# Performance work log

Measured on AMD Instinct MI355X. Metric: run time of the kernel, lower is better.

The kernel has to match this reference:

```python
import jax, jax.numpy as jnp
import numpy as np

B, N, D = 16, 1369, 1024
HID, NH = 512, 8
SCALE = np.sqrt(D // NH)


def _pos_encoding_2d(n, d):
    ps = int(np.sqrt(n))  # 37; n is a perfect square here
    div = jnp.exp(jnp.arange(0, d // 2, 2, dtype=jnp.float32) * (-np.log(10000.0) / (d // 2)))
    rows = (jnp.arange(n) // ps).astype(jnp.float32)
    cols = (jnp.arange(n) % ps).astype(jnp.float32)
    def interleave(s, c):
        return jnp.stack([s, c], axis=-1).reshape(n, -1)
    half_row = interleave(jnp.sin(rows[:, None] * div), jnp.cos(rows[:, None] * div))
    half_col = interleave(jnp.sin(cols[:, None] * div), jnp.cos(cols[:, None] * div))
    return jnp.concatenate([half_row, half_col], axis=-1)  # [n, d]


def _center_bias(n, strength=0.3):
    ps = int(np.sqrt(n))
    c = ps // 2
    y, x = jnp.meshgrid(jnp.arange(ps, dtype=jnp.float32), jnp.arange(ps, dtype=jnp.float32), indexing='ij')
    d2 = (x - c) ** 2 + (y - c) ** 2
    sigma = ps / 6.0
    return (jnp.exp(-d2 / (2.0 * sigma ** 2)).reshape(-1)) * strength  # [n]


def setup_inputs() -> dict:
    key = jax.random.key(0)
    ks = jax.random.split(key, 16)
    s = 0.02
    return {
        'patch_tokens': jax.random.normal(ks[0], (B, N, D), dtype=jnp.float32),
        'curiosity_score': jax.random.uniform(ks[1], (B,), dtype=jnp.float32),
        'Wq': jax.random.normal(ks[2], (D, D), dtype=jnp.float32) * s,
        'bq': jax.random.uniform(ks[3], (D,), minval=-0.05, maxval=0.05, dtype=jnp.float32),
        'Wk': jax.random.normal(ks[4], (D, D), dtype=jnp.float32) * s,
        'bk': jax.random.uniform(ks[5], (D,), minval=-0.05, maxval=0.05, dtype=jnp.float32),
        'Wv': jax.random.normal(ks[6], (D, D), dtype=jnp.float32) * s,
        'bv': jnp.zeros((D,), dtype=jnp.float32),
        'Wc1': jax.random.normal(ks[7], (1, HID // 8), dtype=jnp.float32) * s,
        'bc1': jnp.zeros((HID // 8,), dtype=jnp.float32),
        'Wc2': jax.random.normal(ks[8], (HID // 8, NH), dtype=jnp.float32) * s,
        'bc2': jnp.zeros((NH,), dtype=jnp.float32),
        'Wp1': jax.random.normal(ks[9], (D, HID), dtype=jnp.float32) * s,
        'bp1': jnp.zeros((HID,), dtype=jnp.float32),
        'Wp2': jax.random.normal(ks[10], (HID, HID // 4), dtype=jnp.float32) * s,
        'bp2': jnp.zeros((HID // 4,), dtype=jnp.float32),
        'adaptive_weight': jnp.float32(0.5),
    }


def reference(patch_tokens, curiosity_score, Wq, bq, Wk, bk, Wv, bv,
              Wc1, bc1, Wc2, bc2, Wp1, bp1, Wp2, bp2, adaptive_weight):
    b, n, d = patch_tokens.shape
    x = patch_tokens + _pos_encoding_2d(n, d)[None]  # [B,N,D]

    q = x @ Wq + bq
    k = x @ Wk + bk
    v = x @ Wv + bv

    scores = jnp.einsum('bqd,bkd->bqk', q, k) / SCALE          # [B,N,N]
    attn = jax.nn.softmax(scores, axis=-1)                     # dropout p=0 / eval
    attended = jnp.einsum('bqk,bkd->bqd', attn, v)             # [B,N,D]

    cb = _center_bias(n)[None]                                 # [1,N]
    VAR_EPS = 1e-6

    pa = attn.mean(axis=1) + cb
    # fallback chain (data-dependent in torch; expressed with jnp.where)
    pa2 = jnp.diagonal(attn, axis1=-2, axis2=-1) + cb
    pa = jnp.where(jnp.var(pa, ddof=1) < VAR_EPS, pa2, pa)
    pa3 = attn.max(axis=-1) + cb
    pa = jnp.where(jnp.var(pa, ddof=1) < VAR_EPS, pa3, pa)
    norms = jnp.linalg.norm(x, axis=-1)
    noise = jax.random.normal(jax.random.key(42), norms.shape, dtype=norms.dtype) * 0.1 * jnp.std(norms, ddof=1)
    pa = jnp.where(jnp.var(pa, ddof=1) < VAR_EPS, norms + noise, pa)

    pa = pa / (pa.sum(axis=-1, keepdims=True) + 1e-8)

    # curiosity modulation
    h = jax.nn.relu(curiosity_score[:, None] @ Wc1 + bc1)
    cm = jax.nn.sigmoid(h @ Wc2 + bc2)                         # [B,NH]
    cw = cm.mean(axis=-1, keepdims=True)                       # [B,1]
    modulated = pa * (1.0 + cw)
    fa = adaptive_weight * modulated + (1.0 - adaptive_weight) * pa

    fa = jnp.clip(fa, 1e-8, None)
    fa = fa / (fa.sum(axis=-1, keepdims=True) + 1e-8)

    weighted = jnp.sum(attended * fa[..., None], axis=1)       # [B,D]
    focal = jax.nn.relu(weighted @ Wp1 + bp1) @ Wp2 + bp2      # [B,HID//4]
    return focal, fa
```

## Files before the change

kernel.cpp:

```cpp
#include <hip/hip_runtime.h>
#include <hip/hip_bf16.h>
#include <cstdint>

#define B_   16
#define N_   1369
#define NP   1536
#define D_   1024
#define NQK  2048
#define SLD  1568
#define QLD  2080

typedef __bf16 bf16x8_t __attribute__((ext_vector_type(8)));
typedef __bf16 bf16x4_t __attribute__((ext_vector_type(4)));
typedef float  f32x4_t  __attribute__((ext_vector_type(4)));

__device__ __forceinline__ float  bf2f(__bf16 x) { return (float)x; }
__device__ __forceinline__ __bf16 f2bf(float x)  { return (__bf16)x; }

#define GLOAD_LDS16(g, l) __builtin_amdgcn_global_load_lds( \
    (const __attribute__((address_space(1))) void*)(g),     \
    (__attribute__((address_space(3))) void*)(l), 16, 0, 0)

__global__ __launch_bounds__(256)
void pos_kernel(float* __restrict__ pos)
{
    const int idx = blockIdx.x * 256 + threadIdx.x;
    if (idx >= N_ * D_) return;
    const int n = idx >> 10, f = idx & 1023;
    const int row = n / 37, col = n - row * 37;
    const float base = (f < 512) ? (float)row : (float)col;
    const int  t2   = (f & 511) >> 1;
    const float dv  = __expf(-0.03597789207803197f * (float)t2);
    const float ang = base * dv;
    pos[idx] = (f & 1) ? cosf(ang) : sinf(ang);
}

__global__ __launch_bounds__(256)
void addpos_kernel(const float* __restrict__ patch, const float* __restrict__ pos,
                   __bf16* __restrict__ X)
{
    const long tid = (long)blockIdx.x * 256 + threadIdx.x;
    const long e   = tid * 4;
    const int  f   = (int)(e & 1023);
    const long nb  = e >> 10;
    const int  n   = (int)(nb % NP);
    const long b   = nb / NP;
    bf16x4_t o;
    if (n < N_) {
        const float4 p = *(const float4*)(patch + ((b * N_ + n) << 10) + f);
        const float4 q = *(const float4*)(pos + ((long)n << 10) + f);
        o[0] = f2bf(p.x + q.x); o[1] = f2bf(p.y + q.y);
        o[2] = f2bf(p.z + q.z); o[3] = f2bf(p.w + q.w);
    } else {
        o[0] = o[1] = o[2] = o[3] = f2bf(0.f);
    }
    *(bf16x4_t*)(X + e) = o;
}

__global__ __launch_bounds__(256)
void wcast_kernel(const float* __restrict__ W0, const float* __restrict__ W1,
                  __bf16* __restrict__ T0, __bf16* __restrict__ T1)
{
    const float* W = blockIdx.z == 0 ? W0 : W1;
    __bf16*      T = blockIdx.z == 0 ? T0 : T1;
    __shared__ float tile[64][65];
    const int o0 = blockIdx.x * 64, i0 = blockIdx.y * 64;
    const int t = threadIdx.x;
    const int tr = t >> 4, tc = (t & 15) * 4;
    #pragma unroll
    for (int rr = 0; rr < 64; rr += 16) {
        float4 v = *(const float4*)(W + (long)(i0 + rr + tr) * 1024 + o0 + tc);
        tile[rr + tr][tc + 0] = v.x; tile[rr + tr][tc + 1] = v.y;
        tile[rr + tr][tc + 2] = v.z; tile[rr + tr][tc + 3] = v.w;
    }
    __syncthreads();
    #pragma unroll
    for (int rr = 0; rr < 64; rr += 16) {
        bf16x4_t o;
        o[0] = f2bf(tile[tc + 0][rr + tr]); o[1] = f2bf(tile[tc + 1][rr + tr]);
        o[2] = f2bf(tile[tc + 2][rr + tr]); o[3] = f2bf(tile[tc + 3][rr + tr]);
        *(bf16x4_t*)(T + (long)(o0 + rr + tr) * 1024 + i0 + tc) = o;
    }
}

__global__ __launch_bounds__(256)
void bcat_kernel(const float* __restrict__ bq, const float* __restrict__ bk,
                 float* __restrict__ bcat)
{
    const int i = blockIdx.x * 256 + threadIdx.x;
    if (i >= NQK) return;
    bcat[i] = (i < 1024) ? bq[i] : bk[i - 1024];
}

template<int HAS_BIAS, int STATS>
__device__ __forceinline__
void gemm_body(const __bf16* __restrict__ A, const __bf16* __restrict__ Bt,
               __bf16* __restrict__ C, const float* __restrict__ bias,
               float2* __restrict__ mzp,
               int lda, int ldb, int ldc, int Kd, float scale,
               long sA, long sB, long sC, int tilesN, int tilesPerBatch, int cpx)
{
    __shared__ __bf16 lds[65536];
    const int bid = blockIdx.x;
    const int vt  = (bid & 7) * cpx + (bid >> 3);
    const int bz  = vt / tilesPerBatch;
    const int rem = vt - bz * tilesPerBatch;
    const int ty  = rem / tilesN;
    const int tx  = rem - ty * tilesN;
    A  += (long)bz * sA;  Bt += (long)bz * sB;  C += (long)bz * sC;
    const int m0 = ty * 256, n0 = tx * 256;

    const int t  = threadIdx.x;
    const int w  = t >> 6, l = t & 63;
    const int wr = w >> 2, wc = w & 3;
    const int lr = l & 15, lh = l >> 4;

    const int laneF  = (lr * 64 + ((lh * 16) ^ (((lr >> 3) & 1) << 5))) >> 1;
    const int rstage = (w >> 1) * 16 + (l >> 2);
    const int kstage = (w & 1) * 32 + (((l & 3) * 8) ^ (((l >> 5) & 1) << 4));

    const __bf16* Ag = A  + (long)(m0 + rstage) * lda + kstage;
    const __bf16* Bg = Bt + (long)(n0 + rstage) * ldb + kstage;
    __bf16* dA = lds + w * 512;
    __bf16* dB = lds + 16384 + w * 512;

#define SA_(buf, half, kt) GLOAD_LDS16(Ag + (long)(half) * 128 * lda + (kt) * 64, \
                                       dA + (buf) * 32768 + (half) * 8192)
#define SB_(buf, half, kt) GLOAD_LDS16(Bg + (long)(half) * 128 * ldb + (kt) * 64, \
                                       dB + (buf) * 32768 + (half) * 8192)

    f32x4_t acc[4][4] = {};

    const int NT = Kd >> 6;
    SA_(0, 0, 0); SA_(0, 1, 0); SB_(0, 0, 0); SB_(0, 1, 0);
    asm volatile("s_waitcnt vmcnt(0)" ::: "memory");
    __builtin_amdgcn_s_barrier();

    for (int tk = 0; tk < NT; ++tk) {
        const int c = tk & 1, o = c ^ 1;
        if (tk + 1 < NT) {
            SA_(o, 0, tk + 1); SA_(o, 1, tk + 1);
            SB_(o, 0, tk + 1); SB_(o, 1, tk + 1);
        }
        const int cb = c * 32768;
        const __bf16* ap = lds + cb + (wr >> 1) * 8192 + (wr & 1) * 4096 + laneF;
        const __bf16* bp = lds + cb + 16384 + (wc >> 1) * 8192 + (wc & 1) * 4096 + laneF;
        bf16x8_t af[4], bfm[4];
        #pragma unroll
        for (int nn = 0; nn < 4; ++nn) bfm[nn] = *(const bf16x8_t*)(bp + nn * 1024);
        #pragma unroll
        for (int mi = 0; mi < 4; ++mi) af[mi]  = *(const bf16x8_t*)(ap + mi * 1024);
        __builtin_amdgcn_s_setprio(1);
        #pragma unroll
        for (int mi = 0; mi < 4; ++mi)
            #pragma unroll
            for (int nn = 0; nn < 4; ++nn)
                acc[mi][nn] = __builtin_amdgcn_mfma_f32_16x16x32_bf16(af[mi], bfm[nn], acc[mi][nn], 0, 0, 0);
        __builtin_amdgcn_s_setprio(0);
        #pragma unroll
        for (int nn = 0; nn < 4; ++nn) bfm[nn] = *(const bf16x8_t*)(bp + nn * 1024 + 512);
        #pragma unroll
        for (int mi = 0; mi < 4; ++mi) af[mi]  = *(const bf16x8_t*)(ap + mi * 1024 + 512);
        __builtin_amdgcn_s_setprio(1);
        #pragma unroll
        for (int mi = 0; mi < 4; ++mi)
            #pragma unroll
            for (int nn = 0; nn < 4; ++nn)
                acc[mi][nn] = __builtin_amdgcn_mfma_f32_16x16x32_bf16(af[mi], bfm[nn], acc[mi][nn], 0, 0, 0);
        __builtin_amdgcn_s_setprio(0);
        asm volatile("s_waitcnt vmcnt(0)" ::: "memory");
        __builtin_amdgcn_s_barrier();
    }

    #pragma unroll
    for (int mi = 0; mi < 4; ++mi) {
        const int row = m0 + wr * 64 + mi * 16 + lh * 4;
        #pragma unroll
        for (int nn = 0; nn < 4; ++nn) {
            const int col = n0 + wc * 64 + nn * 16 + lr;
            const float bb = HAS_BIAS ? bias[col] : 0.0f;
            #pragma unroll
            for (int q = 0; q < 4; ++q) {
                if (!STATS || ((row + q) < N_ && col < N_))
                    C[(long)(row + q) * ldc + col] = f2bf(acc[mi][nn][q] * scale + bb);
            }
        }
    }

    if (STATS) {
        __syncthreads();
        float* lm = (float*)lds;
        float* lz = lm + 1024;
        #pragma unroll
        for (int mi = 0; mi < 4; ++mi) {
            #pragma unroll
            for (int qq = 0; qq < 4; ++qq) {
                float vb[4]; float m = -3.0e38f;
                #pragma unroll
                for (int nn = 0; nn < 4; ++nn) {
                    const int col = n0 + wc * 64 + nn * 16 + lr;
                    const float vr = bf2f(f2bf(acc[mi][nn][qq] * scale));
                    vb[nn] = (col < N_) ? vr : -3.0e38f;
                    m = fmaxf(m, vb[nn]);
                }
                #pragma unroll
                for (int o = 1; o <= 8; o <<= 1) m = fmaxf(m, __shfl_xor(m, o));
                float z = 0.f;
                #pragma unroll
                for (int nn = 0; nn < 4; ++nn) z += __expf(vb[nn] - m);
                #pragma unroll
                for (int o = 1; o <= 8; o <<= 1) z += __shfl_xor(z, o);
                if (lr == 0) {
                    const int r = wr * 64 + mi * 16 + lh * 4 + qq;
                    lm[r * 4 + wc] = m; lz[r * 4 + wc] = z;
                }
            }
        }
        __syncthreads();
        if (t < 256) {
            const float ma = lm[t * 4 + 0], mb = lm[t * 4 + 1];
            const float mc = lm[t * 4 + 2], md = lm[t * 4 + 3];
            const float M = fmaxf(fmaxf(ma, mb), fmaxf(mc, md));
            const float Z = lz[t * 4 + 0] * __expf(ma - M) + lz[t * 4 + 1] * __expf(mb - M)
                          + lz[t * 4 + 2] * __expf(mc - M) + lz[t * 4 + 3] * __expf(md - M);
            mzp[((long)bz * NP + ty * 256 + t) * 6 + tx] = make_float2(M, Z);
        }
    }
#undef SA_
#undef SB_
}

__global__ __launch_bounds__(1024, 4)
void gemm_qk(const __bf16* A, const __bf16* Bt, __bf16* C, const float* bias,
             int lda, int ldb, int ldc, int Kd,
             int tilesN, int tilesPerBatch, int cpx)
{
    gemm_body<1, 0>(A, Bt, C, bias, nullptr, lda, ldb, ldc, Kd, 1.0f,
                    0, 0, 0, tilesN, tilesPerBatch, cpx);
}

__global__ __launch_bounds__(1024, 4)
void gemm_sc(const __bf16* A, const __bf16* Bt, __bf16* C, float2* mzp,
             int lda, int ldb, int ldc, int Kd, float scale,
             long sA, long sB, long sC, int tilesN, int tilesPerBatch, int cpx)
{
    gemm_body<0, 1>(A, Bt, C, nullptr, mzp, lda, ldb, ldc, Kd, scale,
                    sA, sB, sC, tilesN, tilesPerBatch, cpx);
}

template<int WEIGHTED>
__global__ __launch_bounds__(256)
void colsum_kernel(const __bf16* __restrict__ attn, const float2* __restrict__ mzp,
                   const float* __restrict__ wv, float* __restrict__ out)
{
    const int t  = threadIdx.x;
    const int b  = blockIdx.y;
    const int q0 = blockIdx.x * 16;
    __shared__ float sM[16], sZi[16];
    if (t < 16) {
        const int q = q0 + t;
        float M = -3.0e38f, Zi = 1.f;
        if (q < N_) {
            float2 p[6];
            #pragma unroll
            for (int k = 0; k < 6; ++k) { p[k] = mzp[((long)b * NP + q) * 6 + k]; M = fmaxf(M, p[k].x); }
            float Z = 0.f;
            #pragma unroll
            for (int k = 0; k < 6; ++k) Z += p[k].y * __expf(p[k].x - M);
            Zi = 1.f / Z;
        }
        sM[t] = M; sZi[t] = Zi;
    }
    __syncthreads();
    const int k8 = t * 8;
    if (k8 < N_) {
        const int q1 = (q0 + 16 < N_) ? q0 + 16 : N_;
        float s[8] = {};
        const __bf16* base = attn + (long)b * NP * SLD + k8;
        for (int q = q0; q < q1; ++q) {
            bf16x8_t v = *(const bf16x8_t*)(base + (long)q * SLD);
            const float Mq = sM[q - q0];
            float wq = sZi[q - q0];
            if (WEIGHTED) wq *= wv[b * NP + q];
            #pragma unroll
            for (int i = 0; i < 8; ++i) s[i] += wq * __expf(bf2f(v[i]) - Mq);
        }
        #pragma unroll
        for (int i = 0; i < 8; ++i) atomicAdd(out + b * NP + k8 + i, s[i]);
    }
}

__global__ __launch_bounds__(256)
void fa_kernel(const float* __restrict__ pa_raw, const float* __restrict__ curiosity,
               const float* __restrict__ Wc1, const float* __restrict__ bc1,
               const float* __restrict__ Wc2, const float* __restrict__ bc2,
               const float* __restrict__ aw_p,
               float* __restrict__ fa_ws, float* __restrict__ out_fa)
{
    const int b = blockIdx.x, t = threadIdx.x;
    __shared__ float hsh[64];
    __shared__ float red[8];
    __shared__ float cwsh;
    if (t < 64) hsh[t] = fmaxf(0.f, curiosity[b] * Wc1[t] + bc1[t]);
    __syncthreads();
    if (t < 8) {
        float a = bc2[t];
        for (int j = 0; j < 64; ++j) a += hsh[j] * Wc2[j * 8 + t];
        red[t] = 1.f / (1.f + __expf(-a));
    }
    __syncthreads();
    if (t == 0) {
        float cw = 0.f;
        for (int i = 0; i < 8; ++i) cw += red[i];
        cwsh = cw * 0.125f;
    }
    __syncthreads();
    const float aw   = aw_p[0];
    const float modf = 1.f + aw * cwsh;
    const float sig  = 37.f / 6.f;
    const float inv2s2 = 1.f / (2.f * sig * sig);
    float pv[6];
    float s1 = 0.f;
    #pragma unroll
    for (int i = 0; i < 6; ++i) {
        const int k = t + i * 256;
        float p = 0.f;
        if (k < N_) {
            const int y = k / 37, x = k - y * 37;
            const float d2 = (float)((x - 18) * (x - 18) + (y - 18) * (y - 18));
            const float cb = 0.3f * __expf(-d2 * inv2s2);
            p = pa_raw[b * NP + k] * (1.f / 1369.f) + cb;
        }
        pv[i] = p; s1 += p;
    }
    #pragma unroll
    for (int o = 32; o; o >>= 1) s1 += __shfl_xor(s1, o);
    __syncthreads();
    if (!(t & 63)) red[t >> 6] = s1;
    __syncthreads();
    s1 = red[0] + red[1] + red[2] + red[3];
    const float inv1 = 1.f / (s1 + 1e-8f);
    float s2 = 0.f;
    #pragma unroll
    for (int i = 0; i < 6; ++i) {
        const int k = t + i * 256;
        if (k < N_) {
            const float f = fmaxf(pv[i] * inv1 * modf, 1e-8f);
            pv[i] = f; s2 += f;
        }
    }
    #pragma unroll
    for (int o = 32; o; o >>= 1) s2 += __shfl_xor(s2, o);
    if (!(t & 63)) red[4 + (t >> 6)] = s2;
    __syncthreads();
    s2 = red[4] + red[5] + red[6] + red[7];
    const float inv2 = 1.f / (s2 + 1e-8f);
    #pragma unroll
    for (int i = 0; i < 6; ++i) {
        const int k = t + i * 256;
        if (k < N_) {
            const float f = pv[i] * inv2;
            fa_ws[b * NP + k]  = f;
            out_fa[b * N_ + k] = f;
        }
    }
}

__global__ __launch_bounds__(256)
void u_kernel(const float* __restrict__ g, const __bf16* __restrict__ X,
              float* __restrict__ u, float* __restrict__ gsum)
{
    const int b  = blockIdx.y;
    const int k0 = blockIdx.x * 86;
    const int k1 = (k0 + 86 < N_) ? k0 + 86 : N_;
    const int d  = threadIdx.x * 4;
    float a0 = 0, a1 = 0, a2 = 0, a3 = 0, gs = 0;
    const __bf16* xb = X + (long)b * NP * D_ + d;
    for (int k = k0; k < k1; ++k) {
        const float gv = g[b * NP + k];
        bf16x4_t xv = *(const bf16x4_t*)(xb + (long)k * D_);
        a0 += gv * bf2f(xv[0]); a1 += gv * bf2f(xv[1]);
        a2 += gv * bf2f(xv[2]); a3 += gv * bf2f(xv[3]);
        gs += gv;
    }
    atomicAdd(u + b * D_ + d + 0, a0);
    atomicAdd(u + b * D_ + d + 1, a1);
    atomicAdd(u + b * D_ + d + 2, a2);
    atomicAdd(u + b * D_ + d + 3, a3);
    if (threadIdx.x == 0) atomicAdd(gsum + b, gs);
}

__global__ __launch_bounds__(256)
void wv_gemv_kernel(const float* __restrict__ u, const float* __restrict__ gsum,
                    const float* __restrict__ Wv, const float* __restrict__ bv,
                    float* __restrict__ wout)
{
    const int dcx = blockIdx.x, b = blockIdx.y;
    const int t = threadIdx.x;
    __shared__ float us[1024];
    #pragma unroll
    for (int i = 0; i < 4; ++i) us[t + i * 256] = u[b * D_ + t + i * 256];
    __syncthreads();
    const int d = dcx * 256 + t;
    float a = gsum[b] * bv[d];
    #pragma unroll 8
    for (int i = 0; i < 1024; ++i) a += us[i] * Wv[(long)i * 1024 + d];
    wout[b * D_ + d] = a;
}

__global__ __launch_bounds__(256)
void focal1_kernel(const float* __restrict__ weighted, const float* __restrict__ Wp1,
                   const float* __restrict__ bp1, float* __restrict__ h)
{
    const int b = blockIdx.y, jc = blockIdx.x;
    const int t = threadIdx.x;
    const int jl = t >> 2, part = t & 3;
    const int j = jc * 64 + jl;
    const float* wb = weighted + b * 1024 + part * 256;
    const float* wp = Wp1 + (long)(part * 256) * 512 + j;
    float a = 0.f;
    #pragma unroll 8
    for (int d = 0; d < 256; ++d) a += wb[d] * wp[(long)d * 512];
    a += __shfl_xor(a, 1);
    a += __shfl_xor(a, 2);
    if (part == 0) h[b * 512 + j] = fmaxf(a + bp1[j], 0.f);
}

__global__ __launch_bounds__(128)
void focal2_kernel(const float* __restrict__ h, const float* __restrict__ Wp2,
                   const float* __restrict__ bp2, float* __restrict__ out)
{
    const int b = blockIdx.x, o = threadIdx.x;
    __shared__ float hs[512];
    for (int i = o; i < 512; i += 128) hs[i] = h[b * 512 + i];
    __syncthreads();
    float a = bp2[o];
    #pragma unroll 8
    for (int j = 0; j < 512; ++j) a += hs[j] * Wp2[j * 128 + o];
    out[b * 128 + o] = a;
}

extern "C" void kernel_launch(void* const* d_in, const int* in_sizes, int n_in,
                              void* d_out, int out_size, void* d_ws, size_t ws_size,
                              hipStream_t stream)
{
    const float* patch     = (const float*)d_in[0];
    const float* curiosity = (const float*)d_in[1];
    const float* Wq  = (const float*)d_in[2];
    const float* bq  = (const float*)d_in[3];
    const float* Wk  = (const float*)d_in[4];
    const float* bk  = (const float*)d_in[5];
    const float* Wv  = (const float*)d_in[6];
    const float* bv  = (const float*)d_in[7];
    const float* Wc1 = (const float*)d_in[8];
    const float* bc1 = (const float*)d_in[9];
    const float* Wc2 = (const float*)d_in[10];
    const float* bc2 = (const float*)d_in[11];
    const float* Wp1 = (const float*)d_in[12];
    const float* bp1 = (const float*)d_in[13];
    const float* Wp2 = (const float*)d_in[14];
    const float* bp2 = (const float*)d_in[15];
    const float* aw  = (const float*)d_in[16];
    float* out = (float*)d_out;

    char* ws = (char*)d_ws;
    size_t off = 0;
    auto alloc = [&](size_t bytes) -> char* {
        char* p = ws + off;
        off += (bytes + 255) & ~(size_t)255;
        return p;
    };
    float*  pos  = (float*) alloc((size_t)N_ * D_ * 4);
    __bf16* X    = (__bf16*)alloc((size_t)B_ * NP * D_ * 2);
    __bf16* WT   = (__bf16*)alloc((size_t)2 * D_ * D_ * 2);
    __bf16* S    = (__bf16*)alloc((size_t)B_ * NP * SLD * 2);
    __bf16* QK   = (__bf16*)alloc((size_t)B_ * NP * QLD * 2);
    float*  pa   = (float*) alloc((size_t)B_ * NP * 4);
    float*  gbuf = (float*) alloc((size_t)B_ * NP * 4);
    float*  ubuf = (float*) alloc((size_t)B_ * D_ * 4);
    float*  gsum = (float*) alloc((size_t)B_ * 4);
    const size_t zbytes = (size_t)((char*)(gsum + B_) - (char*)pa);
    float*  faw  = (float*) alloc((size_t)B_ * NP * 4);
    float*  bcat = (float*) alloc((size_t)NQK * 4);
    float*  hbuf = (float*) alloc((size_t)B_ * 512 * 4);
    float2* mzp  = (float2*)alloc((size_t)B_ * NP * 6 * 8);
    float*  wsum = (float*) alloc((size_t)B_ * D_ * 4);

    (void)hipMemsetAsync(pa, 0, zbytes, stream);

    pos_kernel<<<(N_ * D_ + 255) / 256, 256, 0, stream>>>(pos);
    addpos_kernel<<<(int)((size_t)B_ * NP * D_ / 4 / 256), 256, 0, stream>>>(patch, pos, X);
    {
        dim3 g(16, 16, 2);
        wcast_kernel<<<g, 256, 0, stream>>>(Wq, Wk, WT, WT + D_ * D_);
    }
    bcat_kernel<<<(NQK + 255) / 256, 256, 0, stream>>>(bq, bk, bcat);
    {
        const int nwg = 96 * 8;
        gemm_qk<<<nwg, 1024, 0, stream>>>(X, WT, QK, bcat,
                                          D_, D_, QLD, D_, 8, nwg, nwg / 8);
    }
    {
        const int nwg = 36 * B_;
        gemm_sc<<<nwg, 1024, 0, stream>>>(QK, QK + 1024, S, mzp,
                                          QLD, QLD, SLD, D_,
                                          0.08838834764831845f,
                                          (long)NP * QLD, (long)NP * QLD,
                                          (long)NP * SLD, 6, 36, nwg / 8);
    }
    {
        dim3 g(86, B_);
        colsum_kernel<0><<<g, 256, 0, stream>>>(S, mzp, nullptr, pa);
    }
    fa_kernel<<<B_, 256, 0, stream>>>(pa, curiosity, Wc1, bc1, Wc2, bc2, aw,
                                      faw, out + B_ * 128);
    {
        dim3 g(86, B_);
        colsum_kernel<1><<<g, 256, 0, stream>>>(S, mzp, faw, gbuf);
    }
    {
        dim3 g(16, B_);
        u_kernel<<<g, 256, 0, stream>>>(gbuf, X, ubuf, gsum);
    }
    {
        dim3 g(4, B_);
        wv_gemv_kernel<<<g, 256, 0, stream>>>(ubuf, gsum, Wv, bv, wsum);
    }
    {
        dim3 g(8, B_);
        focal1_kernel<<<g, 256, 0, stream>>>(wsum, Wp1, bp1, hbuf);
    }
    focal2_kernel<<<B_, 128, 0, stream>>>(hbuf, Wp2, bp2, out);
}
```

Baseline: 551.3 us.

## Drop softmax max-subtraction via atomic row sums and halve GEMM K-tile

The score GEMM no longer computes per-tile row max and partition pairs. Instead it accumulates plain exp sums directly into a per-row Z buffer with atomics, and the colsum kernels use exp(v)/Z with no max shift. The GEMM K-step also drops from 64 to 32, which halves LDS use and may allow more blocks per CU. The risk is overflow in exp if scores grow large, since the stable max shift is gone. The smaller K step also doubles the barrier count per output tile.

Result: slower. 567.0 us (+2.9%).

```diff
diff --git a/kernel.cpp b/kernel.cpp
--- a/kernel.cpp
+++ b/kernel.cpp
@@ -96,11 +96,11 @@
 __device__ __forceinline__
 void gemm_body(const __bf16* __restrict__ A, const __bf16* __restrict__ Bt,
                __bf16* __restrict__ C, const float* __restrict__ bias,
-               float2* __restrict__ mzp,
+               float* __restrict__ rowZ,
                int lda, int ldb, int ldc, int Kd, float scale,
                long sA, long sB, long sC, int tilesN, int tilesPerBatch, int cpx)
 {
-    __shared__ __bf16 lds[65536];
+    __shared__ __bf16 lds[32768];
     const int bid = blockIdx.x;
     const int vt  = (bid & 7) * cpx + (bid >> 3);
     const int bz  = vt / tilesPerBatch;
@@ -115,52 +115,36 @@
     const int wr = w >> 2, wc = w & 3;
     const int lr = l & 15, lh = l >> 4;
 
-    const int laneF  = (lr * 64 + ((lh * 16) ^ (((lr >> 3) & 1) << 5))) >> 1;
-    const int rstage = (w >> 1) * 16 + (l >> 2);
-    const int kstage = (w & 1) * 32 + (((l & 3) * 8) ^ (((l >> 5) & 1) << 4));
+    const int laneF  = lr * 32 + ((lh * 8) ^ (((lr >> 3) & 1) << 4));
+    const int rstage = w * 16 + (l >> 2);
+    const int kstage = ((l & 3) * 8) ^ (((l >> 5) & 1) << 4);
 
     const __bf16* Ag = A  + (long)(m0 + rstage) * lda + kstage;
     const __bf16* Bg = Bt + (long)(n0 + rstage) * ldb + kstage;
     __bf16* dA = lds + w * 512;
-    __bf16* dB = lds + 16384 + w * 512;
-
-#define SA_(buf, half, kt) GLOAD_LDS16(Ag + (long)(half) * 128 * lda + (kt) * 64, \
-                                       dA + (buf) * 32768 + (half) * 8192)
-#define SB_(buf, half, kt) GLOAD_LDS16(Bg + (long)(half) * 128 * ldb + (kt) * 64, \
-                                       dB + (buf) * 32768 + (half) * 8192)
+    __bf16* dB = lds + 8192 + w * 512;
+
+#define SA_(buf, kt) GLOAD_LDS16(Ag + (kt) * 32, dA + (buf) * 16384)
+#define SB_(buf, kt) GLOAD_LDS16(Bg + (kt) * 32, dB + (buf) * 16384)
 
     f32x4_t acc[4][4] = {};
 
-    const int NT = Kd >> 6;
-    SA_(0, 0, 0); SA_(0, 1, 0); SB_(0, 0, 0); SB_(0, 1, 0);
+    const int NT = Kd >> 5;
+    SA_(0, 0); SB_(0, 0);
     asm volatile("s_waitcnt vmcnt(0)" ::: "memory");
     __builtin_amdgcn_s_barrier();
 
     for (int tk = 0; tk < NT; ++tk) {
         const int c = tk & 1, o = c ^ 1;
-        if (tk + 1 < NT) {
-            SA_(o, 0, tk + 1); SA_(o, 1, tk + 1);
-            SB_(o, 0, tk + 1); SB_(o, 1, tk + 1);
-        }
-        const int cb = c * 32768;
-        const __bf16* ap = lds + cb + (wr >> 1) * 8192 + (wr & 1) * 4096 + laneF;
-        const __bf16* bp = lds + cb + 16384 + (wc >> 1) * 8192 + (wc & 1) * 4096 + laneF;
+        if (tk + 1 < NT) { SA_(o, tk + 1); SB_(o, tk + 1); }
+        const int cb = c * 16384;
+        const __bf16* ap = lds + cb + wr * 2048 + laneF;
+        const __bf16* bp = lds + cb + 8192 + wc * 2048 + laneF;
         bf16x8_t af[4], bfm[4];
         #pragma unroll
-        for (int nn = 0; nn < 4; ++nn) bfm[nn] = *(const bf16x8_t*)(bp + nn * 1024);
-        #pragma unroll
-        for (int mi = 0; mi < 4; ++mi) af[mi]  = *(const bf16x8_t*)(ap + mi * 1024);
-        __builtin_amdgcn_s_setprio(1);
-        #pragma unroll
-        for (int mi = 0; mi < 4; ++mi)
-            #pragma unroll
-            for (int nn = 0; nn < 4; ++nn)
-                acc[mi][nn] = __builtin_amdgcn_mfma_f32_16x16x32_bf16(af[mi], bfm[nn], acc[mi][nn], 0, 0, 0);
-        __builtin_amdgcn_s_setprio(0);
-        #pragma unroll
-        for (int nn = 0; nn < 4; ++nn) bfm[nn] = *(const bf16x8_t*)(bp + nn * 1024 + 512);
-        #pragma unroll
-        for (int mi = 0; mi < 4; ++mi) af[mi]  = *(const bf16x8_t*)(ap + mi * 1024 + 512);
+        for (int nn = 0; nn < 4; ++nn) bfm[nn] = *(const bf16x8_t*)(bp + nn * 512);
+        #pragma unroll
+        for (int mi = 0; mi < 4; ++mi) af[mi]  = *(const bf16x8_t*)(ap + mi * 512);
         __builtin_amdgcn_s_setprio(1);
         #pragma unroll
         for (int mi = 0; mi < 4; ++mi)
@@ -188,42 +172,23 @@
     }
 
     if (STATS) {
-        __syncthreads();
-        float* lm = (float*)lds;
-        float* lz = lm + 1024;
         #pragma unroll
         for (int mi = 0; mi < 4; ++mi) {
             #pragma unroll
             for (int qq = 0; qq < 4; ++qq) {
-                float vb[4]; float m = -3.0e38f;
+                float z = 0.f;
                 #pragma unroll
                 for (int nn = 0; nn < 4; ++nn) {
                     const int col = n0 + wc * 64 + nn * 16 + lr;
                     const float vr = bf2f(f2bf(acc[mi][nn][qq] * scale));
-                    vb[nn] = (col < N_) ? vr : -3.0e38f;
-                    m = fmaxf(m, vb[nn]);
+                    if (col < N_) z += __expf(vr);
                 }
                 #pragma unroll
-                for (int o = 1; o <= 8; o <<= 1) m = fmaxf(m, __shfl_xor(m, o));
-                float z = 0.f;
-                #pragma unroll
-                for (int nn = 0; nn < 4; ++nn) z += __expf(vb[nn] - m);
-                #pragma unroll
-                for (int o = 1; o <= 8; o <<= 1) z += __shfl_xor(z, o);
-                if (lr == 0) {
-                    const int r = wr * 64 + mi * 16 + lh * 4 + qq;
-                    lm[r * 4 + wc] = m; lz[r * 4 + wc] = z;
-                }
+                for (int o2 = 1; o2 <= 8; o2 <<= 1) z += __shfl_xor(z, o2);
+                const int r = ty * 256 + wr * 64 + mi * 16 + lh * 4 + qq;
+                if (lr == 0 && r < N_)
+                    atomicAdd(rowZ + (long)bz * NP + r, z);
             }
-        }
-        __syncthreads();
-        if (t < 256) {
-            const float ma = lm[t * 4 + 0], mb = lm[t * 4 + 1];
-            const float mc = lm[t * 4 + 2], md = lm[t * 4 + 3];
-            const float M = fmaxf(fmaxf(ma, mb), fmaxf(mc, md));
-            const float Z = lz[t * 4 + 0] * __expf(ma - M) + lz[t * 4 + 1] * __expf(mb - M)
-                          + lz[t * 4 + 2] * __expf(mc - M) + lz[t * 4 + 3] * __expf(md - M);
-            mzp[((long)bz * NP + ty * 256 + t) * 6 + tx] = make_float2(M, Z);
         }
     }
 #undef SA_
@@ -240,36 +205,31 @@
 }
 
 __global__ __launch_bounds__(1024, 4)
-void gemm_sc(const __bf16* A, const __bf16* Bt, __bf16* C, float2* mzp,
+void gemm_sc(const __bf16* A, const __bf16* Bt, __bf16* C, float* rowZ,
              int lda, int ldb, int ldc, int Kd, float scale,
              long sA, long sB, long sC, int tilesN, int tilesPerBatch, int cpx)
 {
-    gemm_body<0, 1>(A, Bt, C, nullptr, mzp, lda, ldb, ldc, Kd, scale,
+    gemm_body<0, 1>(A, Bt, C, nullptr, rowZ, lda, ldb, ldc, Kd, scale,
                     sA, sB, sC, tilesN, tilesPerBatch, cpx);
 }
 
 template<int WEIGHTED>
 __global__ __launch_bounds__(256)
-void colsum_kernel(const __bf16* __restrict__ attn, const float2* __restrict__ mzp,
+void colsum_kernel(const __bf16* __restrict__ attn, const float* __restrict__ rowZ,
                    const float* __restrict__ wv, float* __restrict__ out)
 {
     const int t  = threadIdx.x;
     const int b  = blockIdx.y;
     const int q0 = blockIdx.x * 16;
-    __shared__ float sM[16], sZi[16];
+    __shared__ float sZi[16];
     if (t < 16) {
         const int q = q0 + t;
-        float M = -3.0e38f, Zi = 1.f;
+        float wq = 0.f;
         if (q < N_) {
-            float2 p[6];
-            #pragma unroll
-            for (int k = 0; k < 6; ++k) { p[k] = mzp[((long)b * NP + q) * 6 + k]; M = fmaxf(M, p[k].x); }
-            float Z = 0.f;
-            #pragma unroll
-            for (int k = 0; k < 6; ++k) Z += p[k].y * __expf(p[k].x - M);
-            Zi = 1.f / Z;
-        }
-        sM[t] = M; sZi[t] = Zi;
+            wq = 1.f / rowZ[(long)b * NP + q];
+            if (WEIGHTED) wq *= wv[b * NP + q];
+        }
+        sZi[t] = wq;
     }
     __syncthreads();
     const int k8 = t * 8;
@@ -279,11 +239,9 @@
         const __bf16* base = attn + (long)b * NP * SLD + k8;
         for (int q = q0; q < q1; ++q) {
             bf16x8_t v = *(const bf16x8_t*)(base + (long)q * SLD);
-            const float Mq = sM[q - q0];
-            float wq = sZi[q - q0];
-            if (WEIGHTED) wq *= wv[b * NP + q];
+            const float wq = sZi[q - q0];
             #pragma unroll
-            for (int i = 0; i < 8; ++i) s[i] += wq * __expf(bf2f(v[i]) - Mq);
+            for (int i = 0; i < 8; ++i) s[i] += wq * __expf(bf2f(v[i]));
         }
         #pragma unroll
         for (int i = 0; i < 8; ++i) atomicAdd(out + b * NP + k8 + i, s[i]);
@@ -479,11 +437,11 @@
     float*  gbuf = (float*) alloc((size_t)B_ * NP * 4);
     float*  ubuf = (float*) alloc((size_t)B_ * D_ * 4);
     float*  gsum = (float*) alloc((size_t)B_ * 4);
-    const size_t zbytes = (size_t)((char*)(gsum + B_) - (char*)pa);
+    float*  rowZ = (float*) alloc((size_t)B_ * NP * 4);
+    const size_t zbytes = (size_t)((char*)(rowZ + B_ * NP) - (char*)pa);
     float*  faw  = (float*) alloc((size_t)B_ * NP * 4);
     float*  bcat = (float*) alloc((size_t)NQK * 4);
     float*  hbuf = (float*) alloc((size_t)B_ * 512 * 4);
-    float2* mzp  = (float2*)alloc((size_t)B_ * NP * 6 * 8);
     float*  wsum = (float*) alloc((size_t)B_ * D_ * 4);
 
     (void)hipMemsetAsync(pa, 0, zbytes, stream);
@@ -502,7 +460,7 @@
     }
     {
         const int nwg = 36 * B_;
-        gemm_sc<<<nwg, 1024, 0, stream>>>(QK, QK + 1024, S, mzp,
+        gemm_sc<<<nwg, 1024, 0, stream>>>(QK, QK + 1024, S, rowZ,
                                           QLD, QLD, SLD, D_,
                                           0.08838834764831845f,
                                           (long)NP * QLD, (long)NP * QLD,
@@ -510,13 +468,13 @@
     }
     {
         dim3 g(86, B_);
-        colsum_kernel<0><<<g, 256, 0, stream>>>(S, mzp, nullptr, pa);
+        colsum_kernel<0><<<g, 256, 0, stream>>>(S, rowZ, nullptr, pa);
     }
     fa_kernel<<<B_, 256, 0, stream>>>(pa, curiosity, Wc1, bc1, Wc2, bc2, aw,
                                       faw, out + B_ * 128);
     {
         dim3 g(86, B_);
-        colsum_kernel<1><<<g, 256, 0, stream>>>(S, mzp, faw, gbuf);
+        colsum_kernel<1><<<g, 256, 0, stream>>>(S, rowZ, faw, gbuf);
     }
     {
         dim3 g(16, B_);
```
